# Kernel tuning notes

Measured on AMD Instinct MI355X. Metric: run time of the kernel, lower is better.

Reference implementation:

```python
import jax, jax.numpy as jnp
import numpy as np

EPS_NORM = 1e-12   # F.normalize eps
EPS_Q = 1e-5       # quant scale clamp

def simple_rmsnorm(x):
    # F.normalize(x, dim=-1) * sqrt(dim)  ==  x / sqrt(mean(x^2))
    d = x.shape[-1]
    n = jnp.maximum(jnp.linalg.norm(x, axis=-1, keepdims=True), EPS_NORM)
    return x / n * jnp.sqrt(jnp.asarray(d, x.dtype))

def activation_quant(x):
    # per-token 8-bit absmax quant
    scale = 127.0 / jnp.clip(jnp.max(jnp.abs(x), axis=-1, keepdims=True), EPS_Q, None)
    return jnp.clip(jnp.round(x * scale), -128.0, 127.0) / scale

def weight_quant(w):
    # per-tensor ternary quant: scale = 1 / mean|w|
    scale = 1.0 / jnp.clip(jnp.mean(jnp.abs(w)), EPS_Q, None)
    return jnp.clip(jnp.round(w * scale), -1.0, 1.0) / scale

def bitlinear158(x, w):
    xn = simple_rmsnorm(x)
    # straight-through estimators
    xq = xn + jax.lax.stop_gradient(activation_quant(xn) - xn)
    wq = w + jax.lax.stop_gradient(weight_quant(w) - w)
    # w is [out, in] like nn.Linear
    return jnp.einsum('bsd,od->bso', xq, wq)

def setup_inputs() -> dict:
    key = jax.random.key(0)
    k1, k2, k3 = jax.random.split(key, 3)
    dim, inner = 2048, 8192
    x = jax.random.normal(k1, (4, 2048, dim), dtype=jnp.float32)
    w1 = jax.random.normal(k2, (inner, dim), dtype=jnp.float32) * 0.02
    w2 = jax.random.normal(k3, (dim, inner), dtype=jnp.float32) * 0.02
    return {"x": x, "w1": w1, "w2": w2}

def reference(x, w1, w2):
    h = bitlinear158(x, w1)
    h = jax.nn.gelu(h, approximate=False)  # nn.GELU() default = exact erf
    return bitlinear158(h, w2)
```

## Files before the change

kernel.cpp:

```cpp
#include <hip/hip_runtime.h>
#include <hip/hip_bf16.h>
#include <hip/hip_fp16.h>

typedef __attribute__((ext_vector_type(4))) int i32x4;
typedef __attribute__((ext_vector_type(8))) unsigned short u16x8;
typedef __attribute__((ext_vector_type(8))) char c8;
typedef __attribute__((ext_vector_type(4))) char c4;
typedef unsigned int u32;
typedef unsigned short u16;

#define SCH0() __builtin_amdgcn_sched_barrier(0)

__device__ __forceinline__ void gload_lds16(const void* g, void* l) {
  __builtin_amdgcn_global_load_lds((const u32 __attribute__((address_space(1)))*)g,
                                   (u32 __attribute__((address_space(3)))*)l, 16, 0, 0);
}
__device__ __forceinline__ float h2f(u16 u) { return __half2float(__ushort_as_half(u)); }
__device__ __forceinline__ u16  f2h(float f){ return __half_as_ushort(__float2half_rn(f)); }

__global__ __launch_bounds__(256) void quant_x_kernel(const float* __restrict__ x,
    char* __restrict__ qx, float* __restrict__ invs) {
  const int D = 2048;
  int row = blockIdx.x, tid = threadIdx.x;
  const float* xr = x + (size_t)row * D;
  float4 a = ((const float4*)xr)[tid * 2], b = ((const float4*)xr)[tid * 2 + 1];
  float v[8] = {a.x, a.y, a.z, a.w, b.x, b.y, b.z, b.w};
  double ss = 0; float mx = 0.0f;
#pragma unroll
  for (int i = 0; i < 8; i++) { ss += (double)v[i] * v[i]; mx = fmaxf(mx, fabsf(v[i])); }
  __shared__ double sd[256]; __shared__ float sf[256];
  sd[tid] = ss; sf[tid] = mx; __syncthreads();
  for (int o = 128; o > 0; o >>= 1) {
    if (tid < o) { sd[tid] += sd[tid + o]; sf[tid] = fmaxf(sf[tid], sf[tid + o]); }
    __syncthreads();
  }
  __shared__ float bn, bs;
  if (tid == 0) {
    float n = fmaxf((float)sqrt(sd[0]), 1e-12f);
    float amax = sf[0] * (sqrtf((float)D) / n);
    float cl = fmaxf(amax, 1e-5f);
    bn = n; bs = 127.0f / cl;
    invs[row] = cl / 127.0f;
  }
  __syncthreads();
  float n = bn, s = bs, sq = sqrtf((float)D);
  c8 q;
#pragma unroll
  for (int i = 0; i < 8; i++) {
    float xn = (v[i] / n) * sq;
    float r = rintf(xn * s);
    r = fminf(fmaxf(r, -128.0f), 127.0f);
    q[i] = (char)(int)r;
  }
  *(c8*)&qx[(size_t)row * D + tid * 8] = q;
}

__global__ __launch_bounds__(256) void absum_partial(const float* __restrict__ w,
    double* __restrict__ part, int n4) {
  int tid = threadIdx.x;
  double s = 0;
  for (int i = blockIdx.x * 256 + tid; i < n4; i += gridDim.x * 256) {
    float4 v = ((const float4*)w)[i];
    s += (double)fabsf(v.x) + (double)fabsf(v.y) + (double)fabsf(v.z) + (double)fabsf(v.w);
  }
  __shared__ double sd[256];
  sd[tid] = s; __syncthreads();
  for (int o = 128; o > 0; o >>= 1) { if (tid < o) sd[tid] += sd[tid + o]; __syncthreads(); }
  if (tid == 0) part[blockIdx.x] = sd[0];
}

__global__ __launch_bounds__(256) void wscale_final(const double* __restrict__ part,
    float* __restrict__ wsc) {
  int tid = threadIdx.x;
  __shared__ double sd[256];
  sd[tid] = part[tid] + part[tid + 256]; __syncthreads();
  for (int o = 128; o > 0; o >>= 1) { if (tid < o) sd[tid] += sd[tid + o]; __syncthreads(); }
  double s1 = sd[0]; __syncthreads();
  sd[tid] = part[512 + tid] + part[768 + tid]; __syncthreads();
  for (int o = 128; o > 0; o >>= 1) { if (tid < o) sd[tid] += sd[tid + o]; __syncthreads(); }
  if (tid == 0) {
    float m1 = (float)(s1 / 16777216.0);
    float m2 = (float)(sd[0] / 16777216.0);
    float d1 = fmaxf(m1, 1e-5f), d2 = fmaxf(m2, 1e-5f);
    wsc[0] = 1.0f / d1; wsc[1] = d1; wsc[2] = 1.0f / d2; wsc[3] = d2;
  }
}

__global__ __launch_bounds__(256) void quant_w_kernel(const float* __restrict__ w,
    char* __restrict__ q, const float* __restrict__ wsc, int widx, int n4) {
  float s = wsc[widx];
  for (int i = blockIdx.x * 256 + threadIdx.x; i < n4; i += gridDim.x * 256) {
    float4 v = ((const float4*)w)[i];
    c4 o;
    o[0] = (char)(int)(fminf(fmaxf(rintf(v.x * s), -1.0f), 1.0f));
    o[1] = (char)(int)(fminf(fmaxf(rintf(v.y * s), -1.0f), 1.0f));
    o[2] = (char)(int)(fminf(fmaxf(rintf(v.z * s), -1.0f), 1.0f));
    o[3] = (char)(int)(fminf(fmaxf(rintf(v.w * s), -1.0f), 1.0f));
    ((c4*)q)[i] = o;
  }
}

template <int EPI>
__global__ __launch_bounds__(512, 2) void gemm_i8(const char* __restrict__ A,
    const char* __restrict__ B, int N, int K, size_t ldA, size_t ldB, int gridN,
    const float* __restrict__ rowscale, const float* __restrict__ wsc,
    int widx, void* __restrict__ outp) {
  __shared__ __align__(16) char sm[3][2][16384];
  const int tid = threadIdx.x;
  const int lane = tid & 63, w = tid >> 6;
  const int wm = w >> 2, wn = w & 3;
  const int llo = lane & 15, lhi = lane >> 4;
  const int koff = ((lhi ^ ((llo >> 1) & 3)) << 4);

  const int nwg = gridDim.x, cpx = nwg >> 3;
  const int swz = (blockIdx.x & 7) * cpx + (blockIdx.x >> 3);
  const int bm = swz / gridN, bn = swz % gridN;

  const int NT = K >> 6;
  const size_t Abase = (size_t)(bm * 256) * ldA;
  const size_t Bbase = (size_t)(bn * 256) * ldB;

  const int rs = tid >> 2;
  const int kbs = (((tid & 3) ^ ((tid >> 3) & 3)) << 4);

  auto stage = [&](int mat, int buf, int hf, int kt) {
    const char* G = (mat == 0) ? A : B;
    size_t ld = (mat == 0) ? ldA : ldB;
    size_t base = (mat == 0) ? Abase : Bbase;
    gload_lds16(G + base + (size_t)(hf * 128 + rs) * ld + (size_t)kt * 64 + kbs,
                &sm[buf][mat][hf * 8192 + tid * 16]);
  };
  auto stage_tile = [&](int buf, int kt) {
    stage(0, buf, 0, kt); stage(1, buf, 0, kt);
    stage(0, buf, 1, kt); stage(1, buf, 1, kt);
  };

  i32x4 alo[4], ahi[4], blo[2], bhi[2];
  auto readA = [&](int buf, int half, i32x4 (&dst)[4]) {
    int rbase = wm * 128 + half * 64 + llo;
#pragma unroll
    for (int f = 0; f < 4; f++)
      dst[f] = *(const i32x4*)&sm[buf][0][(rbase + f * 16) * 64 + koff];
  };
  auto readB = [&](int buf, int half, i32x4 (&dst)[2]) {
    int rbase = wn * 64 + half * 32 + llo;
#pragma unroll
    for (int f = 0; f < 2; f++)
      dst[f] = *(const i32x4*)&sm[buf][1][(rbase + f * 16) * 64 + koff];
  };

  i32x4 acc[8][4];
#pragma unroll
  for (int m = 0; m < 8; m++)
#pragma unroll
    for (int n = 0; n < 4; n++) acc[m][n] = (i32x4){0, 0, 0, 0};

  auto mmaq = [&](i32x4 (&av)[4], i32x4 (&bv)[2], int mh, int nh) {
    __builtin_amdgcn_s_setprio(1);
#pragma unroll
    for (int m = 0; m < 4; m++)
#pragma unroll
      for (int n = 0; n < 2; n++)
        acc[mh * 4 + m][nh * 2 + n] =
            __builtin_amdgcn_mfma_i32_16x16x64_i8(av[m], bv[n],
                                                  acc[mh * 4 + m][nh * 2 + n], 0, 0, 0);
    __builtin_amdgcn_s_setprio(0);
  };

  stage_tile(0, 0);
  asm volatile("s_nop 0" ::: "memory");
  stage_tile(1, 1);

  int bR = 0, bS = 2;
  for (int t = 0; t < NT; t++) {
    if (t + 1 < NT) asm volatile("s_waitcnt vmcnt(4)\n\ts_barrier" ::: "memory");
    else            asm volatile("s_waitcnt vmcnt(0)\n\ts_barrier" ::: "memory");
    if (t + 2 < NT) stage_tile(bS, t + 2);
    SCH0();
    readA(bR, 0, alo); readB(bR, 0, blo);
    readB(bR, 1, bhi);
    mmaq(alo, blo, 0, 0);
    readA(bR, 1, ahi);
    mmaq(alo, bhi, 0, 1);
    mmaq(ahi, blo, 1, 0);
    mmaq(ahi, bhi, 1, 1);
    bR = (bR == 2) ? 0 : bR + 1;
    bS = (bS == 2) ? 0 : bS + 1;
  }

  float wdeq = wsc[widx];
#pragma unroll
  for (int mf = 0; mf < 8; mf++) {
#pragma unroll
    for (int reg = 0; reg < 4; reg++) {
      int r = bm * 256 + wm * 128 + mf * 16 + lhi * 4 + reg;
      float deq = rowscale[r] * wdeq;
#pragma unroll
      for (int nf = 0; nf < 4; nf++) {
        int c = bn * 256 + wn * 64 + nf * 16 + llo;
        float val = (float)acc[mf][nf][reg] * deq;
        if (EPI == 0) {
          float g = 0.5f * val * (1.0f + erff(val * 0.70710678118654752440f));
          ((u16*)outp)[(size_t)r * N + c] = f2h(g);
        } else {
          ((float*)outp)[(size_t)r * N + c] = val;
        }
      }
    }
  }
}

__global__ __launch_bounds__(256) void quant_h_kernel(u16* __restrict__ h, float* __restrict__ invs) {
  const int D = 8192;
  int row = blockIdx.x, tid = threadIdx.x;
  u16* hr = h + (size_t)row * D;
  float v[32];
#pragma unroll
  for (int j = 0; j < 4; j++) {
    u16x8 u = *(const u16x8*)&hr[j * 2048 + tid * 8];
#pragma unroll
    for (int e = 0; e < 8; e++) v[j * 8 + e] = h2f(u[e]);
  }
  double ss = 0; float mx = 0.0f;
#pragma unroll
  for (int i = 0; i < 32; i++) { ss += (double)v[i] * v[i]; mx = fmaxf(mx, fabsf(v[i])); }
  __shared__ double sd[256]; __shared__ float sf[256];
  sd[tid] = ss; sf[tid] = mx; __syncthreads();
  for (int o = 128; o > 0; o >>= 1) {
    if (tid < o) { sd[tid] += sd[tid + o]; sf[tid] = fmaxf(sf[tid], sf[tid + o]); }
    __syncthreads();
  }
  __shared__ float bn, bs;
  if (tid == 0) {
    float n = fmaxf((float)sqrt(sd[0]), 1e-12f);
    float amax = sf[0] * (sqrtf((float)D) / n);
    float cl = fmaxf(amax, 1e-5f);
    bn = n; bs = 127.0f / cl;
    invs[row] = cl / 127.0f;
  }
  __syncthreads();
  float n = bn, s = bs, sq = sqrtf((float)D);
  char* hq = (char*)hr;
#pragma unroll
  for (int j = 0; j < 4; j++) {
    c8 q;
#pragma unroll
    for (int e = 0; e < 8; e++) {
      float xn = (v[j * 8 + e] / n) * sq;
      float r = rintf(xn * s);
      r = fminf(fmaxf(r, -128.0f), 127.0f);
      q[e] = (char)(int)r;
    }
    *(c8*)&hq[j * 2048 + tid * 8] = q;
  }
}

extern "C" void kernel_launch(void* const* d_in, const int* in_sizes, int n_in,
                              void* d_out, int out_size, void* d_ws, size_t ws_size,
                              hipStream_t stream) {
  const float* x  = (const float*)d_in[0];
  const float* w1 = (const float*)d_in[1];
  const float* w2 = (const float*)d_in[2];

  char* ws = (char*)d_ws;
  char*   qx     = (char*)(ws + 0);
  char*   w1q    = (char*)(ws + 16777216);
  char*   w2q    = (char*)(ws + 33554432);
  u16*    h      = (u16*)(ws + 50331648);
  float*  invs_x = (float*)(ws + 184549376);
  float*  invs_h = (float*)(ws + 184582144);
  double* part   = (double*)(ws + 184614912);
  float*  wsc    = (float*)(ws + 184623104);

  quant_x_kernel<<<8192, 256, 0, stream>>>(x, qx, invs_x);
  absum_partial<<<512, 256, 0, stream>>>(w1, part, 4194304);
  absum_partial<<<512, 256, 0, stream>>>(w2, part + 512, 4194304);
  wscale_final<<<1, 256, 0, stream>>>(part, wsc);
  quant_w_kernel<<<2048, 256, 0, stream>>>(w1, w1q, wsc, 0, 4194304);
  quant_w_kernel<<<2048, 256, 0, stream>>>(w2, w2q, wsc, 2, 4194304);
  gemm_i8<0><<<1024, 512, 0, stream>>>(qx, w1q, 8192, 2048, 2048, 2048, 32,
                                       invs_x, wsc, 1, (void*)h);
  quant_h_kernel<<<8192, 256, 0, stream>>>(h, invs_h);
  gemm_i8<1><<<256, 512, 0, stream>>>((const char*)h, w2q, 2048, 8192, 16384, 8192, 8,
                                      invs_h, wsc, 3, d_out);
}
```

Baseline: 455.5 us.

## Shrink int8 GEMM tiles to 128x128 with double buffering and 4 waves

Replaces the 256x256-tile, 8-wave, triple-buffered int8 MFMA GEMM with a 128x128-tile, 4-wave, double-buffered version and launches four times as many workgroups. Each wave now loads all of its A/B fragments at once and issues 16 MFMAs per k-step. An extra barrier after the LDS reads protects buffer reuse. The aim is more workgroups per CU and better load balance, especially for the second GEMM, which previously had only 256 workgroups. The cost is lower data reuse per tile, which means more global and LDS traffic, and less latency hiding with only two buffers.

```diff
diff --git a/kernel.cpp b/kernel.cpp
--- a/kernel.cpp
+++ b/kernel.cpp
@@ -101,14 +101,14 @@
 }
 
 template <int EPI>
-__global__ __launch_bounds__(512, 2) void gemm_i8(const char* __restrict__ A,
+__global__ __launch_bounds__(256, 4) void gemm128(const char* __restrict__ A,
     const char* __restrict__ B, int N, int K, size_t ldA, size_t ldB, int gridN,
     const float* __restrict__ rowscale, const float* __restrict__ wsc,
     int widx, void* __restrict__ outp) {
-  __shared__ __align__(16) char sm[3][2][16384];
+  __shared__ __align__(16) char sm[2][2][8192];
   const int tid = threadIdx.x;
   const int lane = tid & 63, w = tid >> 6;
-  const int wm = w >> 2, wn = w & 3;
+  const int wm = w >> 1, wn = w & 1;
   const int llo = lane & 15, lhi = lane >> 4;
   const int koff = ((lhi ^ ((llo >> 1) & 3)) << 4);
 
@@ -117,87 +117,71 @@
   const int bm = swz / gridN, bn = swz % gridN;
 
   const int NT = K >> 6;
-  const size_t Abase = (size_t)(bm * 256) * ldA;
-  const size_t Bbase = (size_t)(bn * 256) * ldB;
-
-  const int rs = tid >> 2;
-  const int kbs = (((tid & 3) ^ ((tid >> 3) & 3)) << 4);
-
-  auto stage = [&](int mat, int buf, int hf, int kt) {
-    const char* G = (mat == 0) ? A : B;
-    size_t ld = (mat == 0) ? ldA : ldB;
-    size_t base = (mat == 0) ? Abase : Bbase;
-    gload_lds16(G + base + (size_t)(hf * 128 + rs) * ld + (size_t)kt * 64 + kbs,
-                &sm[buf][mat][hf * 8192 + tid * 16]);
+  const size_t Abase = (size_t)(bm * 128) * ldA;
+  const size_t Bbase = (size_t)(bn * 128) * ldB;
+
+  const int r0 = tid >> 2;
+  const int kb0 = (((tid & 3) ^ ((tid >> 3) & 3)) << 4);
+
+  auto stage_tile = [&](int buf, int kt) {
+    size_t ko = (size_t)kt * 64;
+    gload_lds16(A + Abase + (size_t)r0 * ldA + ko + kb0,        &sm[buf][0][tid * 16]);
+    gload_lds16(A + Abase + (size_t)(64 + r0) * ldA + ko + kb0, &sm[buf][0][4096 + tid * 16]);
+    gload_lds16(B + Bbase + (size_t)r0 * ldB + ko + kb0,        &sm[buf][1][tid * 16]);
+    gload_lds16(B + Bbase + (size_t)(64 + r0) * ldB + ko + kb0, &sm[buf][1][4096 + tid * 16]);
   };
-  auto stage_tile = [&](int buf, int kt) {
-    stage(0, buf, 0, kt); stage(1, buf, 0, kt);
-    stage(0, buf, 1, kt); stage(1, buf, 1, kt);
+
+  i32x4 a[4], b[4];
+  auto readAB = [&](int buf) {
+    int ra = wm * 64 + llo, rb = wn * 64 + llo;
+#pragma unroll
+    for (int f = 0; f < 4; f++)
+      a[f] = *(const i32x4*)&sm[buf][0][(ra + f * 16) * 64 + koff];
+#pragma unroll
+    for (int f = 0; f < 4; f++)
+      b[f] = *(const i32x4*)&sm[buf][1][(rb + f * 16) * 64 + koff];
   };
 
-  i32x4 alo[4], ahi[4], blo[2], bhi[2];
-  auto readA = [&](int buf, int half, i32x4 (&dst)[4]) {
-    int rbase = wm * 128 + half * 64 + llo;
-#pragma unroll
-    for (int f = 0; f < 4; f++)
-      dst[f] = *(const i32x4*)&sm[buf][0][(rbase + f * 16) * 64 + koff];
-  };
-  auto readB = [&](int buf, int half, i32x4 (&dst)[2]) {
-    int rbase = wn * 64 + half * 32 + llo;
-#pragma unroll
-    for (int f = 0; f < 2; f++)
-      dst[f] = *(const i32x4*)&sm[buf][1][(rbase + f * 16) * 64 + koff];
-  };
-
-  i32x4 acc[8][4];
-#pragma unroll
-  for (int m = 0; m < 8; m++)
+  i32x4 acc[4][4];
+#pragma unroll
+  for (int m = 0; m < 4; m++)
 #pragma unroll
     for (int n = 0; n < 4; n++) acc[m][n] = (i32x4){0, 0, 0, 0};
-
-  auto mmaq = [&](i32x4 (&av)[4], i32x4 (&bv)[2], int mh, int nh) {
-    __builtin_amdgcn_s_setprio(1);
-#pragma unroll
-    for (int m = 0; m < 4; m++)
-#pragma unroll
-      for (int n = 0; n < 2; n++)
-        acc[mh * 4 + m][nh * 2 + n] =
-            __builtin_amdgcn_mfma_i32_16x16x64_i8(av[m], bv[n],
-                                                  acc[mh * 4 + m][nh * 2 + n], 0, 0, 0);
-    __builtin_amdgcn_s_setprio(0);
-  };
 
   stage_tile(0, 0);
   asm volatile("s_nop 0" ::: "memory");
   stage_tile(1, 1);
-
-  int bR = 0, bS = 2;
+  asm volatile("s_waitcnt vmcnt(4)\n\ts_barrier" ::: "memory");
+
   for (int t = 0; t < NT; t++) {
-    if (t + 1 < NT) asm volatile("s_waitcnt vmcnt(4)\n\ts_barrier" ::: "memory");
-    else            asm volatile("s_waitcnt vmcnt(0)\n\ts_barrier" ::: "memory");
-    if (t + 2 < NT) stage_tile(bS, t + 2);
+    const int cur = t & 1;
+    readAB(cur);
+    asm volatile("s_waitcnt lgkmcnt(0)\n\ts_barrier" ::: "memory");
+    if (t + 2 < NT) stage_tile(cur, t + 2);
     SCH0();
-    readA(bR, 0, alo); readB(bR, 0, blo);
-    readB(bR, 1, bhi);
-    mmaq(alo, blo, 0, 0);
-    readA(bR, 1, ahi);
-    mmaq(alo, bhi, 0, 1);
-    mmaq(ahi, blo, 1, 0);
-    mmaq(ahi, bhi, 1, 1);
-    bR = (bR == 2) ? 0 : bR + 1;
-    bS = (bS == 2) ? 0 : bS + 1;
+    __builtin_amdgcn_s_setprio(1);
+#pragma unroll
+    for (int m = 0; m < 4; m++)
+#pragma unroll
+      for (int n = 0; n < 4; n++)
+        acc[m][n] = __builtin_amdgcn_mfma_i32_16x16x64_i8(a[m], b[n], acc[m][n], 0, 0, 0);
+    __builtin_amdgcn_s_setprio(0);
+    if (t + 1 < NT) {
+      if (t + 2 < NT) asm volatile("s_waitcnt vmcnt(4)\n\ts_barrier" ::: "memory");
+      else            asm volatile("s_waitcnt vmcnt(0)\n\ts_barrier" ::: "memory");
+    }
   }
 
   float wdeq = wsc[widx];
 #pragma unroll
-  for (int mf = 0; mf < 8; mf++) {
+  for (int mf = 0; mf < 4; mf++) {
 #pragma unroll
     for (int reg = 0; reg < 4; reg++) {
-      int r = bm * 256 + wm * 128 + mf * 16 + lhi * 4 + reg;
+      int r = bm * 128 + wm * 64 + mf * 16 + lhi * 4 + reg;
       float deq = rowscale[r] * wdeq;
 #pragma unroll
       for (int nf = 0; nf < 4; nf++) {
-        int c = bn * 256 + wn * 64 + nf * 16 + llo;
+        int c = bn * 128 + wn * 64 + nf * 16 + llo;
         float val = (float)acc[mf][nf][reg] * deq;
         if (EPI == 0) {
           float g = 0.5f * val * (1.0f + erff(val * 0.70710678118654752440f));
@@ -278,9 +262,9 @@
   wscale_final<<<1, 256, 0, stream>>>(part, wsc);
   quant_w_kernel<<<2048, 256, 0, stream>>>(w1, w1q, wsc, 0, 4194304);
   quant_w_kernel<<<2048, 256, 0, stream>>>(w2, w2q, wsc, 2, 4194304);
-  gemm_i8<0><<<1024, 512, 0, stream>>>(qx, w1q, 8192, 2048, 2048, 2048, 32,
+  gemm128<0><<<4096, 256, 0, stream>>>(qx, w1q, 8192, 2048, 2048, 2048, 64,
                                        invs_x, wsc, 1, (void*)h);
   quant_h_kernel<<<8192, 256, 0, stream>>>(h, invs_h);
-  gemm_i8<1><<<256, 512, 0, stream>>>((const char*)h, w2q, 2048, 8192, 16384, 8192, 8,
-                                      invs_h, wsc, 3, d_out);
-}
+  gemm128<1><<<1024, 256, 0, stream>>>((const char*)h, w2q, 2048, 8192, 16384, 8192, 16,
+                                       invs_h, wsc, 3, d_out);
+}
```

Result: slower. 489.4 us (+7.4%).
